# Performance work log

Measured on AMD Instinct MI355X. Metric: run time of the kernel, lower is better.

## Reference

```python
import jax, jax.numpy as jnp
import numpy as np

N = 50000   # nodes
E = 800000  # edges (avg degree 16)
G = 64      # graphs in batch
H = 4       # attention heads
D = 128     # hidden dim per head (= hidden_dim)
V = 128     # embedding vocab (input_dim)
NEG_SLOPE = 0.2

def setup_inputs() -> dict:
    key = jax.random.key(0)
    ks = jax.random.split(key, 12)
    s = 0.05
    return {
        "feats": jax.random.randint(ks[0], (N,), 0, V),
        "src": jax.random.randint(ks[1], (E,), 0, N),
        "dst": jax.random.randint(ks[2], (E,), 0, N),
        "graph_ids": jnp.sort(jax.random.randint(ks[3], (N,), 0, G)),
        "emb": jax.random.normal(ks[4], (V, D)) * s,
        "W1": jax.random.normal(ks[5], (D, H * D)) * s,
        "b1": jax.random.normal(ks[6], (H * D,)) * s,
        "a1": jax.random.normal(ks[7], (H, D)) * s,
        "W2": jax.random.normal(ks[8], (D, H * D)) * s,
        "b2": jax.random.normal(ks[9], (H * D,)) * s,
        "a2": jax.random.normal(ks[10], (H, D)) * s,
        "Wreg": jax.random.normal(ks[11], (1, D)) * s,
    }

def gatv2_layer(x, W, b, a, src, dst):
    # shared-weight GATv2: h = Wx + b, split into heads -> [N,H,D]
    h = (x @ W + b).reshape(-1, H, D)
    hs = h[src]                      # [E,H,D] source feats per edge
    hd = h[dst]                      # [E,H,D] dest feats per edge
    e = jax.nn.leaky_relu(hs + hd, NEG_SLOPE)
    logits = jnp.einsum('ehd,hd->eh', e, a)          # [E,H]
    # edge softmax over incoming edges of each dst node
    m = jax.ops.segment_max(logits, dst, num_segments=N)
    m = jnp.where(jnp.isfinite(m), m, 0.0)           # empty segments -> 0 (unused)
    ex = jnp.exp(logits - m[dst])
    denom = jax.ops.segment_sum(ex, dst, num_segments=N)
    alpha = ex / denom[dst]                          # [E,H]
    rst = jax.ops.segment_sum(alpha[:, :, None] * hs, dst, num_segments=N)  # [N,H,D]
    return rst.mean(axis=1)          # .mean(dim=1) over heads -> [N,D]

def reference(feats, src, dst, graph_ids, emb, W1, b1, a1, W2, b2, a2, Wreg):
    x = emb[feats]                                   # embedding lookup [N,D]
    x = gatv2_layer(x, W1, b1, a1, src, dst)         # layer 1 (dropout=0)
    x = gatv2_layer(x, W2, b2, a2, src, dst)         # layer 2
    pooled = jax.ops.segment_sum(x, graph_ids, num_segments=G)  # SumPooling [G,D]
    return pooled @ Wreg.T                           # Linear bias=False -> [G,1]
```

## Files before the change

### kernel.cpp

```cpp
#include <hip/hip_runtime.h>
#include <hip/hip_bf16.h>

#define N_NODES 50000
#define N_EDGES 800000
#define G_GRAPHS 64
#define H_HEADS 4
#define D_DIM 128
#define HD 512
#define V_VOCAB 128
#define NEG_SLOPE 0.2f

typedef float f32x2v __attribute__((ext_vector_type(2)));
typedef float f32x4 __attribute__((ext_vector_type(4)));
typedef short s16x8 __attribute__((ext_vector_type(8)));
typedef _Float16 h16x2 __attribute__((ext_vector_type(2)));

static __device__ __forceinline__ unsigned short f2b(float f) {
    union { float f; unsigned int i; } x; x.f = f;
    unsigned int r = x.i + 0x7fffu + ((x.i >> 16) & 1u);
    return (unsigned short)(r >> 16);
}
static __device__ __forceinline__ h16x2 u2h2(unsigned int u) {
    union { unsigned int u; h16x2 h; } c; c.u = u; return c.h;
}
static __device__ __forceinline__ unsigned int h22u(h16x2 h) {
    union { unsigned int u; h16x2 h; } c; c.h = h; return c.u;
}
static __device__ __forceinline__ h16x2 packf2(float lo, float hi) {
    union { __fp16 __attribute__((ext_vector_type(2))) p; h16x2 h; } c;
    c.p = __builtin_amdgcn_cvt_pkrtz(lo, hi);
    return c.h;
}

#if __has_builtin(__builtin_amdgcn_cvt_scalef32_pk_f16_fp8)
static __device__ __forceinline__ void fp8x4_to_h16(unsigned int u, h16x2& h0, h16x2& h1) {
    auto r0 = __builtin_amdgcn_cvt_scalef32_pk_f16_fp8((int)u, 1.0f, false);
    auto r1 = __builtin_amdgcn_cvt_scalef32_pk_f16_fp8((int)u, 1.0f, true);
    union { decltype(r0) p; h16x2 h; } c0, c1;
    c0.p = r0; c1.p = r1;
    h0 = c0.h; h1 = c1.h;
}
#else
static __device__ __forceinline__ void fp8x4_to_h16(unsigned int u, h16x2& h0, h16x2& h1) {
    f32x2v lo = __builtin_amdgcn_cvt_pk_f32_fp8(u, false);
    f32x2v hi = __builtin_amdgcn_cvt_pk_f32_fp8(u, true);
    h0 = packf2(lo.x, lo.y);
    h1 = packf2(hi.x, hi.y);
}
#endif

template<int CTRL>
static __device__ __forceinline__ float dpp_add(float v) {
    union { float f; int i; } a, b;
    a.f = v;
    b.i = __builtin_amdgcn_mov_dpp(a.i, CTRL, 0xF, 0xF, true);
    return v + b.f;
}
static __device__ __forceinline__ float row16_sum(float p) {
    p = dpp_add<0xB1>(p);
    p = dpp_add<0x4E>(p);
    p = dpp_add<0x141>(p);
    p = dpp_add<0x140>(p);
    return p;
}

#define MEGA_M1_BLOCKS   64
#define MEGA_WSZ_BLOCKS  256
#define MEGA_HIST_BLOCKS ((N_EDGES + 255) / 256)
__global__ void __launch_bounds__(256) mega_kernel(const float* __restrict__ emb,
                                                   const float* __restrict__ W1,
                                                   const float* __restrict__ b1,
                                                   unsigned int* __restrict__ M1b,
                                                   const float* __restrict__ W2,
                                                   unsigned short* __restrict__ Wb,
                                                   const int* __restrict__ dst,
                                                   int* __restrict__ counts,
                                                   float* __restrict__ pool) {
    int b = blockIdx.x;
    if (b < MEGA_M1_BLOCKS) {
        int idx = b * 256 + threadIdx.x;
        int v = idx >> 7, c0 = (idx & 127) * 4;
        float acc[4] = {b1[c0], b1[c0 + 1], b1[c0 + 2], b1[c0 + 3]};
        for (int k = 0; k < 128; k++) {
            float e = emb[v * 128 + k];
            #pragma unroll
            for (int j = 0; j < 4; j++) acc[j] = fmaf(e, W1[k * 512 + c0 + j], acc[j]);
        }
        unsigned int pk = __builtin_amdgcn_cvt_pk_fp8_f32(acc[0], acc[1], 0, false);
        pk = __builtin_amdgcn_cvt_pk_fp8_f32(acc[2], acc[3], pk, true);
        M1b[idx] = pk;
    } else if (b < MEGA_M1_BLOCKS + MEGA_WSZ_BLOCKS) {
        int idx = (b - MEGA_M1_BLOCKS) * 256 + threadIdx.x;
        int j = idx & 7, c = (idx >> 3) & 511, qq = idx >> 12;
        Wb[idx] = f2b(W2[(qq * 8 + j) * 512 + c]);
    } else {
        int hb = b - MEGA_M1_BLOCKS - MEGA_WSZ_BLOCKS;
        if (hb == 0 && threadIdx.x < G_GRAPHS) pool[threadIdx.x] = 0.f;
        int i = hb * 256 + threadIdx.x;
        if (i < N_EDGES) atomicAdd(&counts[dst[i]], 1);
    }
}

__global__ void __launch_bounds__(256) wtab_kernel(const unsigned int* __restrict__ M1b,
                                                   const float* __restrict__ a,
                                                   float* __restrict__ Wtab) {
    int wid = threadIdx.x >> 6, lane = threadIdx.x & 63;
    int pid = blockIdx.x * 4 + wid;
    int fd = pid >> 7, fs = pid & 127;
    int voff = lane * 2;

    h16x2 a06[4], a04[4], hd2[4], hs[4];
    float4 av0 = *reinterpret_cast<const float4*>(&a[lane * 8]);
    float4 av1 = *reinterpret_cast<const float4*>(&a[lane * 8 + 4]);
    float aa[8] = {av0.x, av0.y, av0.z, av0.w, av1.x, av1.y, av1.z, av1.w};
    const float L2E = 1.4426950408889634f;
    #pragma unroll
    for (int k = 0; k < 4; k++) {
        a06[k][0] = (_Float16)(aa[2*k]   * (0.6f * L2E));
        a06[k][1] = (_Float16)(aa[2*k+1] * (0.6f * L2E));
        a04[k][0] = (_Float16)(aa[2*k]   * (0.4f * L2E));
        a04[k][1] = (_Float16)(aa[2*k+1] * (0.4f * L2E));
    }
    uint2 hv = *reinterpret_cast<const uint2*>(&M1b[(unsigned)fd * 128u + voff]);
    fp8x4_to_h16(hv.x, hd2[0], hd2[1]);
    fp8x4_to_h16(hv.y, hd2[2], hd2[3]);
    uint2 sv = *reinterpret_cast<const uint2*>(&M1b[(unsigned)fs * 128u + voff]);
    fp8x4_to_h16(sv.x, hs[0], hs[1]);
    fp8x4_to_h16(sv.y, hs[2], hs[3]);

    float p = 0.f;
    #pragma unroll
    for (int k = 0; k < 4; k++) {
        h16x2 t2 = hs[k] + hd2[k];
        h16x2 at2 = u2h2(h22u(t2) & 0x7FFF7FFFu);
        p = __builtin_amdgcn_fdot2(t2, a06[k], p, false);
        p = __builtin_amdgcn_fdot2(at2, a04[k], p, false);
    }
    p = row16_sum(p);
    const float C1 = 0.69314718f, C2 = 0.24022651f, C3 = 0.05550411f;
    float w = fmaf(p, fmaf(p, fmaf(p, C3, C2), C1), 1.f);
    if ((lane & 15) == 0) Wtab[pid * 4 + (lane >> 4)] = w;
}

__global__ void __launch_bounds__(256) scanf_kernel(const int* __restrict__ counts,
                                                    int* __restrict__ offsets,
                                                    int* __restrict__ cursor,
                                                    int* __restrict__ bsum,
                                                    int* __restrict__ flag) {
    __shared__ int buf[256];
    __shared__ int sbase;
    int t = threadIdx.x, b = blockIdx.x;
    int i0 = (b * 256 + t) * 4;
    int v[4], c[4], s = 0;
    #pragma unroll
    for (int j = 0; j < 4; j++) {
        int idx = i0 + j;
        v[j] = (idx < N_NODES) ? counts[idx] : 0;
        s += v[j];
        c[j] = s;
    }
    buf[t] = s;
    __syncthreads();
    for (int off = 1; off < 256; off <<= 1) {
        int add = (t >= off) ? buf[t - off] : 0;
        __syncthreads();
        buf[t] += add;
        __syncthreads();
    }
    int ebase = (t > 0) ? buf[t - 1] : 0;
    if (t == 0) {
        bsum[b] = buf[255];
        __threadfence();
        atomicAdd(flag, 1);
        while (atomicAdd(flag, 0) < 64) __builtin_amdgcn_s_sleep(8);
    }
    __syncthreads();
    if (t < 64) {
        int vv = (t < b) ? atomicAdd(&bsum[t], 0) : 0;
        #pragma unroll
        for (int off = 1; off < 64; off <<= 1) vv += __shfl_xor(vv, off);
        if (t == 0) sbase = vv;
    }
    __syncthreads();
    int base = sbase;
    #pragma unroll
    for (int j = 0; j < 4; j++) {
        int idx = i0 + j;
        if (idx < N_NODES) {
            int e = base + ebase + c[j];
            offsets[idx + 1] = e;
            cursor[idx] = e - v[j];
        }
    }
    if (b == 0 && t == 0) offsets[0] = 0;
}

__global__ void scatter_kernel(const int* __restrict__ src, const int* __restrict__ dst,
                               int* __restrict__ cursor, int* __restrict__ csr_src) {
    int i = blockIdx.x * blockDim.x + threadIdx.x;
    if (i < N_EDGES) {
        int d = dst[i];
        int pos = atomicAdd(&cursor[d], 1);
        csr_src[pos] = src[i];
    }
}

template<bool LAYER1>
__global__ void __launch_bounds__(256) gat_kernel(const unsigned int* __restrict__ h,
                                                  const int* __restrict__ offsets,
                                                  const int* __restrict__ csr_src,
                                                  const int* __restrict__ feats,
                                                  const float* __restrict__ a,
                                                  const float* __restrict__ wreg,
                                                  const float* __restrict__ Wtab,
                                                  unsigned short* __restrict__ x,
                                                  float* __restrict__ dots) {
    int wid = threadIdx.x >> 6;
    int lane = threadIdx.x & 63;
    int n = blockIdx.x * 4 + wid;
    if (n >= N_NODES) return;
    n = __builtin_amdgcn_readfirstlane(n);
    int row_s = __builtin_amdgcn_readfirstlane(offsets[n]);
    int row_e = __builtin_amdgcn_readfirstlane(offsets[n + 1]);
    int cnt = row_e - row_s;
    int voff = lane * 2;

    auto ldrow = [&](int s) {
        return *reinterpret_cast<const uint2*>(&h[(unsigned)s * 128u + voff]);
    };

    if constexpr (LAYER1) {
        int fd = __builtin_amdgcn_readfirstlane(feats[n]);
        const float* wrow = &Wtab[fd * 512];
        int woff = lane >> 4;
        h16x2 acc2[4];
        #pragma unroll
        for (int k = 0; k < 4; k++) { acc2[k][0] = (_Float16)0.f; acc2[k][1] = (_Float16)0.f; }
        float den = 0.f;

        auto proc = [&](uint2 sv, float wv) {
            h16x2 hs[4];
            fp8x4_to_h16(sv.x, hs[0], hs[1]);
            fp8x4_to_h16(sv.y, hs[2], hs[3]);
            den += wv;
            h16x2 w2 = packf2(wv, wv);
            #pragma unroll
            for (int k = 0; k < 4; k++) acc2[k] = w2 * hs[k] + acc2[k];
        };

        for (int base = 0; base < cnt; base += 64) {
            int m = min(64, cnt - base);
            int ev = 0;
            if (lane < m) ev = feats[csr_src[row_s + base + lane]];
            int s0 = __builtin_amdgcn_readlane(ev, 0);
            int s1 = __builtin_amdgcn_readlane(ev, m > 1 ? 1 : 0);
            uint2 rA = ldrow(s0), rB = ldrow(s1);
            float wA = wrow[s0 * 4 + woff], wB = wrow[s1 * 4 + woff];
            for (int i = 0; i < m; i += 2) {
                {
                    uint2 c = rA; float wc = wA;
                    int sn = __builtin_amdgcn_readlane(ev, min(i + 2, m - 1));
                    rA = ldrow(sn); wA = wrow[sn * 4 + woff];
                    proc(c, wc);
                }
                if (i + 1 < m) {
                    uint2 c = rB; float wc = wB;
                    int sn = __builtin_amdgcn_readlane(ev, min(i + 3, m - 1));
                    rB = ldrow(sn); wB = wrow[sn * 4 + woff];
                    proc(c, wc);
                }
            }
        }

        float inv = (den > 0.f) ? 0.25f / den : 0.f;
        float out8[8];
        #pragma unroll
        for (int j = 0; j < 8; j++) {
            float r = (float)acc2[j >> 1][j & 1] * inv;
            r += __shfl_xor(r, 16);
            r += __shfl_xor(r, 32);
            out8[j] = r;
        }
        if (lane < 16) {
            union { unsigned short u[8]; uint4 v; } o;
            #pragma unroll
            for (int j = 0; j < 8; j++) o.u[j] = f2b(out8[j]);
            *reinterpret_cast<uint4*>(&x[(unsigned)n * 128u + lane * 8]) = o.v;
        }
        return;
    } else {
        h16x2 hd2[4], a06[4], a04[4], acc2[4];
        float pd;
        {
            uint2 hv = ldrow(n);
            fp8x4_to_h16(hv.x, hd2[0], hd2[1]);
            fp8x4_to_h16(hv.y, hd2[2], hd2[3]);
            float4 av0 = *reinterpret_cast<const float4*>(&a[lane * 8]);
            float4 av1 = *reinterpret_cast<const float4*>(&a[lane * 8 + 4]);
            float aa[8] = {av0.x, av0.y, av0.z, av0.w, av1.x, av1.y, av1.z, av1.w};
            const float L2E = 1.4426950408889634f;
            #pragma unroll
            for (int k = 0; k < 4; k++) {
                a06[k][0] = (_Float16)(aa[2*k]   * (0.6f * L2E));
                a06[k][1] = (_Float16)(aa[2*k+1] * (0.6f * L2E));
                a04[k][0] = (_Float16)(aa[2*k]   * (0.4f * L2E));
                a04[k][1] = (_Float16)(aa[2*k+1] * (0.4f * L2E));
                acc2[k][0] = (_Float16)0.f; acc2[k][1] = (_Float16)0.f;
            }
            float s = 0.f;
            #pragma unroll
            for (int k = 0; k < 4; k++) s = __builtin_amdgcn_fdot2(hd2[k], a06[k], s, false);
            pd = row16_sum(s);
        }

        const float C1 = 0.69314718f, C2 = 0.24022651f, C3 = 0.05550411f;
        float den = 0.f;

        auto process = [&](uint2 sv) {
            h16x2 hs[4];
            fp8x4_to_h16(sv.x, hs[0], hs[1]);
            fp8x4_to_h16(sv.y, hs[2], hs[3]);
            float p0 = 0.f, p1 = 0.f;
            #pragma unroll
            for (int k = 0; k < 2; k++) {
                h16x2 t2 = hs[k] + hd2[k];
                h16x2 at2 = u2h2(h22u(t2) & 0x7FFF7FFFu);
                p0 = __builtin_amdgcn_fdot2(hs[k], a06[k], p0, false);
                p0 = __builtin_amdgcn_fdot2(at2, a04[k], p0, false);
            }
            #pragma unroll
            for (int k = 2; k < 4; k++) {
                h16x2 t2 = hs[k] + hd2[k];
                h16x2 at2 = u2h2(h22u(t2) & 0x7FFF7FFFu);
                p1 = __builtin_amdgcn_fdot2(hs[k], a06[k], p1, false);
                p1 = __builtin_amdgcn_fdot2(at2, a04[k], p1, false);
            }
            float p = row16_sum(p0 + p1) + pd;
            float w = fmaf(p, fmaf(p, fmaf(p, C3, C2), C1), 1.f);
            den += w;
            h16x2 w2 = packf2(w, w);
            #pragma unroll
            for (int k = 0; k < 4; k++) acc2[k] = w2 * hs[k] + acc2[k];
        };

        for (int base = 0; base < cnt; base += 64) {
            int m = min(64, cnt - base);
            int ev = 0;
            if (lane < m) ev = csr_src[row_s + base + lane];
            int s0 = __builtin_amdgcn_readlane(ev, 0);
            int s1 = __builtin_amdgcn_readlane(ev, m > 1 ? 1 : 0);
            uint2 rA = ldrow(s0), rB = ldrow(s1);
            for (int i = 0; i < m; i += 2) {
                {
                    uint2 cur = rA;
                    rA = ldrow(__builtin_amdgcn_readlane(ev, min(i + 2, m - 1)));
                    process(cur);
                }
                if (i + 1 < m) {
                    uint2 cur = rB;
                    rB = ldrow(__builtin_amdgcn_readlane(ev, min(i + 3, m - 1)));
                    process(cur);
                }
            }
        }

        float inv = (den > 0.f) ? 0.25f / den : 0.f;
        float out8[8];
        #pragma unroll
        for (int j = 0; j < 8; j++) {
            float r = (float)acc2[j >> 1][j & 1] * inv;
            r += __shfl_xor(r, 16);
            r += __shfl_xor(r, 32);
            out8[j] = r;
        }
        int d0 = (lane & 15) * 8;
        float4 wv0 = *reinterpret_cast<const float4*>(&wreg[d0]);
        float4 wv1 = *reinterpret_cast<const float4*>(&wreg[d0 + 4]);
        float pdot = out8[0] * wv0.x + out8[1] * wv0.y + out8[2] * wv0.z + out8[3] * wv0.w
                   + out8[4] * wv1.x + out8[5] * wv1.y + out8[6] * wv1.z + out8[7] * wv1.w;
        pdot = row16_sum(pdot);
        if (lane == 0) dots[n] = pdot;
    }
}

__global__ void __launch_bounds__(256) gemm_kernel(const unsigned short* __restrict__ x,
                                                   const unsigned short* __restrict__ Wb,
                                                   const float* __restrict__ bias,
                                                   unsigned char* __restrict__ hout) {
    int w = threadIdx.x >> 6, l = threadIdx.x & 63;
    int rb = blockIdx.y * 64 + w * 16;
    int cb = blockIdx.x * 64;
    int lr = l & 15, lq = l >> 4;
    f32x4 acc[4] = {};
    int arow = rb + lr;
    bool rok = arow < N_NODES;
    #pragma unroll
    for (int s = 0; s < 4; s++) {
        s16x8 afr = {};
        if (rok) afr = *reinterpret_cast<const s16x8*>(&x[(size_t)arow * 128 + s * 32 + lq * 8]);
        #pragma unroll
        for (int sub = 0; sub < 4; sub++) {
            s16x8 bfr = *reinterpret_cast<const s16x8*>(
                &Wb[(((size_t)(s * 4 + lq) * 512) + cb + sub * 16 + lr) << 3]);
            acc[sub] = __builtin_amdgcn_mfma_f32_16x16x32_bf16(bfr, afr, acc[sub], 0, 0, 0);
        }
    }
    if (!rok) return;
    #pragma unroll
    for (int sub = 0; sub < 4; sub++) {
        int col0 = cb + sub * 16 + lq * 4;
        float4 bb = *reinterpret_cast<const float4*>(&bias[col0]);
        unsigned int pk = __builtin_amdgcn_cvt_pk_fp8_f32(acc[sub][0] + bb.x,
                                                          acc[sub][1] + bb.y, 0, false);
        pk = __builtin_amdgcn_cvt_pk_fp8_f32(acc[sub][2] + bb.z,
                                             acc[sub][3] + bb.w, pk, true);
        *reinterpret_cast<unsigned int*>(&hout[(size_t)arow * 512 + col0]) = pk;
    }
}

__global__ void __launch_bounds__(256) pool64_kernel(const float* __restrict__ dots,
                                                     const int* __restrict__ gid,
                                                     float* __restrict__ pool,
                                                     int* __restrict__ done,
                                                     float* __restrict__ out) {
    int wave = (blockIdx.x * blockDim.x + threadIdx.x) >> 6;
    int lane = threadIdx.x & 63;
    int n0 = wave * 64;
    if (n0 < N_NODES) {
        int n = n0 + lane;
        int nc = min(n, N_NODES - 1);
        int g = gid[nc];
        float v = (n < N_NODES) ? dots[n] : 0.f;
        int g0 = __shfl(g, 0);
        bool uni = __all(g == g0);
        if (uni) {
            v += __shfl_xor(v, 1);
            v += __shfl_xor(v, 2);
            v += __shfl_xor(v, 4);
            v += __shfl_xor(v, 8);
            v += __shfl_xor(v, 16);
            v += __shfl_xor(v, 32);
            if (lane == 0) atomicAdd(&pool[g0], v);
        } else {
            if (n < N_NODES) atomicAdd(&pool[g], v);
        }
    }
    __threadfence();
    __syncthreads();
    __shared__ int amlast;
    if (threadIdx.x == 0)
        amlast = (atomicAdd(done, 1) == (int)gridDim.x - 1) ? 1 : 0;
    __syncthreads();
    if (amlast && threadIdx.x < G_GRAPHS) {
        out[threadIdx.x] = atomicAdd(&pool[threadIdx.x], 0.f);
    }
}

extern "C" void kernel_launch(void* const* d_in, const int* in_sizes, int n_in,
                              void* d_out, int out_size, void* d_ws, size_t ws_size,
                              hipStream_t stream) {
    const int* feats = (const int*)d_in[0];
    const int* src   = (const int*)d_in[1];
    const int* dst   = (const int*)d_in[2];
    const int* gids  = (const int*)d_in[3];
    const float* emb  = (const float*)d_in[4];
    const float* W1   = (const float*)d_in[5];
    const float* b1   = (const float*)d_in[6];
    const float* a1   = (const float*)d_in[7];
    const float* W2   = (const float*)d_in[8];
    const float* b2   = (const float*)d_in[9];
    const float* a2   = (const float*)d_in[10];
    const float* wreg = (const float*)d_in[11];
    float* out = (float*)d_out;

    char* ws = (char*)d_ws;
    size_t off = 0;
    auto alloc = [&](size_t bytes) -> void* {
        void* p = ws + off;
        off = (off + bytes + 255) & ~(size_t)255;
        return p;
    };
    int*   counts  = (int*)alloc((size_t)N_NODES * 4 + 8);
    int*   flag    = counts + N_NODES;
    int*   done    = counts + N_NODES + 1;
    int*   offsets = (int*)alloc((size_t)(N_NODES + 1) * 4);
    int*   cursor  = (int*)alloc((size_t)N_NODES * 4);
    int*   csr_src = (int*)alloc((size_t)N_EDGES * 4);
    int*   bsum    = (int*)alloc(64 * 4);
    unsigned int*   M1b = (unsigned int*)alloc((size_t)V_VOCAB * HD);
    unsigned int*   h  = (unsigned int*)alloc((size_t)N_NODES * HD);
    unsigned short* x  = (unsigned short*)alloc((size_t)N_NODES * D_DIM * 2);
    unsigned short* Wb = (unsigned short*)alloc((size_t)D_DIM * HD * 2);
    float* Wtab    = (float*)alloc((size_t)V_VOCAB * V_VOCAB * H_HEADS * 4);
    float* dots    = (float*)alloc((size_t)N_NODES * 4);
    float* pool    = (float*)alloc((size_t)G_GRAPHS * 4);

    hipMemsetAsync(counts, 0, (size_t)N_NODES * 4 + 8, stream);

    mega_kernel<<<MEGA_M1_BLOCKS + MEGA_WSZ_BLOCKS + MEGA_HIST_BLOCKS, 256, 0, stream>>>(
        emb, W1, b1, M1b, W2, Wb, dst, counts, pool);
    wtab_kernel<<<(V_VOCAB * V_VOCAB) / 4, 256, 0, stream>>>(M1b, a1, Wtab);
    scanf_kernel<<<64, 256, 0, stream>>>(counts, offsets, cursor, bsum, flag);
    scatter_kernel<<<(N_EDGES + 255) / 256, 256, 0, stream>>>(src, dst, cursor, csr_src);

    gat_kernel<true><<<(N_NODES + 3) / 4, 256, 0, stream>>>(M1b, offsets, csr_src, feats,
                                                            a1, wreg, Wtab, x, dots);
    gemm_kernel<<<dim3(8, (N_NODES + 63) / 64), 256, 0, stream>>>(x, Wb, b2, (unsigned char*)h);
    gat_kernel<false><<<(N_NODES + 3) / 4, 256, 0, stream>>>(h, offsets, csr_src, feats,
                                                             a2, wreg, Wtab, x, dots);

    pool64_kernel<<<(N_NODES / 64 + 4) / 4, 256, 0, stream>>>(dots, gids, pool, done, out);
}
```

Before: 307.6 us.

## Precompute per-node score and readout projections to shrink layer-2 edge work

```diff
diff --git a/kernel.cpp b/kernel.cpp
--- a/kernel.cpp
+++ b/kernel.cpp
@@ -205,13 +205,50 @@
     }
 }
 
+__global__ void __launch_bounds__(256) pq_kernel(const unsigned int* __restrict__ h,
+                                                 const float* __restrict__ a,
+                                                 const float* __restrict__ wreg,
+                                                 float2* __restrict__ pq) {
+    int wid = threadIdx.x >> 6, lane = threadIdx.x & 63;
+    int n = blockIdx.x * 4 + wid;
+    if (n >= N_NODES) return;
+    int voff = lane * 2;
+    const float L2E = 1.4426950408889634f;
+
+    h16x2 a06[4], wf[4], hs[4];
+    float4 av0 = *reinterpret_cast<const float4*>(&a[lane * 8]);
+    float4 av1 = *reinterpret_cast<const float4*>(&a[lane * 8 + 4]);
+    float aa[8] = {av0.x, av0.y, av0.z, av0.w, av1.x, av1.y, av1.z, av1.w};
+    int d0 = (lane & 15) * 8;
+    float4 wv0 = *reinterpret_cast<const float4*>(&wreg[d0]);
+    float4 wv1 = *reinterpret_cast<const float4*>(&wreg[d0 + 4]);
+    float ww[8] = {wv0.x, wv0.y, wv0.z, wv0.w, wv1.x, wv1.y, wv1.z, wv1.w};
+    #pragma unroll
+    for (int k = 0; k < 4; k++) {
+        a06[k] = packf2(aa[2*k] * (0.6f * L2E), aa[2*k+1] * (0.6f * L2E));
+        wf[k]  = packf2(ww[2*k], ww[2*k+1]);
+    }
+    uint2 hv = *reinterpret_cast<const uint2*>(&h[(unsigned)n * 128u + voff]);
+    fp8x4_to_h16(hv.x, hs[0], hs[1]);
+    fp8x4_to_h16(hv.y, hs[2], hs[3]);
+    float ps = 0.f, q = 0.f;
+    #pragma unroll
+    for (int k = 0; k < 4; k++) {
+        ps = __builtin_amdgcn_fdot2(hs[k], a06[k], ps, false);
+        q  = __builtin_amdgcn_fdot2(hs[k], wf[k], q, false);
+    }
+    ps = row16_sum(ps);
+    q = row16_sum(q);
+    if ((lane & 15) == 0) pq[n * 4 + (lane >> 4)] = make_float2(ps, q);
+}
+
 template<bool LAYER1>
 __global__ void __launch_bounds__(256) gat_kernel(const unsigned int* __restrict__ h,
                                                   const int* __restrict__ offsets,
                                                   const int* __restrict__ csr_src,
                                                   const int* __restrict__ feats,
                                                   const float* __restrict__ a,
-                                                  const float* __restrict__ wreg,
+                                                  const float2* __restrict__ pq,
                                                   const float* __restrict__ Wtab,
                                                   unsigned short* __restrict__ x,
                                                   float* __restrict__ dots) {
@@ -289,7 +326,8 @@
         }
         return;
     } else {
-        h16x2 hd2[4], a06[4], a04[4], acc2[4];
+        int woff = lane >> 4;
+        h16x2 hd2[4], a04[4];
         float pd;
         {
             uint2 hv = ldrow(n);
@@ -300,47 +338,29 @@
             float aa[8] = {av0.x, av0.y, av0.z, av0.w, av1.x, av1.y, av1.z, av1.w};
             const float L2E = 1.4426950408889634f;
             #pragma unroll
-            for (int k = 0; k < 4; k++) {
-                a06[k][0] = (_Float16)(aa[2*k]   * (0.6f * L2E));
-                a06[k][1] = (_Float16)(aa[2*k+1] * (0.6f * L2E));
-                a04[k][0] = (_Float16)(aa[2*k]   * (0.4f * L2E));
-                a04[k][1] = (_Float16)(aa[2*k+1] * (0.4f * L2E));
-                acc2[k][0] = (_Float16)0.f; acc2[k][1] = (_Float16)0.f;
-            }
-            float s = 0.f;
-            #pragma unroll
-            for (int k = 0; k < 4; k++) s = __builtin_amdgcn_fdot2(hd2[k], a06[k], s, false);
-            pd = row16_sum(s);
+            for (int k = 0; k < 4; k++)
+                a04[k] = packf2(aa[2*k] * (0.4f * L2E), aa[2*k+1] * (0.4f * L2E));
+            pd = pq[n * 4 + woff].x;
         }
 
         const float C1 = 0.69314718f, C2 = 0.24022651f, C3 = 0.05550411f;
-        float den = 0.f;
-
-        auto process = [&](uint2 sv) {
+        float den = 0.f, num = 0.f;
+
+        auto process = [&](uint2 sv, float2 pqc) {
             h16x2 hs[4];
             fp8x4_to_h16(sv.x, hs[0], hs[1]);
             fp8x4_to_h16(sv.y, hs[2], hs[3]);
-            float p0 = 0.f, p1 = 0.f;
+            float p04 = 0.f;
             #pragma unroll
-            for (int k = 0; k < 2; k++) {
+            for (int k = 0; k < 4; k++) {
                 h16x2 t2 = hs[k] + hd2[k];
                 h16x2 at2 = u2h2(h22u(t2) & 0x7FFF7FFFu);
-                p0 = __builtin_amdgcn_fdot2(hs[k], a06[k], p0, false);
-                p0 = __builtin_amdgcn_fdot2(at2, a04[k], p0, false);
+                p04 = __builtin_amdgcn_fdot2(at2, a04[k], p04, false);
             }
-            #pragma unroll
-            for (int k = 2; k < 4; k++) {
-                h16x2 t2 = hs[k] + hd2[k];
-                h16x2 at2 = u2h2(h22u(t2) & 0x7FFF7FFFu);
-                p1 = __builtin_amdgcn_fdot2(hs[k], a06[k], p1, false);
-                p1 = __builtin_amdgcn_fdot2(at2, a04[k], p1, false);
-            }
-            float p = row16_sum(p0 + p1) + pd;
+            float p = row16_sum(p04) + pqc.x + pd;
             float w = fmaf(p, fmaf(p, fmaf(p, C3, C2), C1), 1.f);
             den += w;
-            h16x2 w2 = packf2(w, w);
-            #pragma unroll
-            for (int k = 0; k < 4; k++) acc2[k] = w2 * hs[k] + acc2[k];
+            num = fmaf(w, pqc.y, num);
         };
 
         for (int base = 0; base < cnt; base += 64) {
@@ -350,36 +370,27 @@
             int s0 = __builtin_amdgcn_readlane(ev, 0);
             int s1 = __builtin_amdgcn_readlane(ev, m > 1 ? 1 : 0);
             uint2 rA = ldrow(s0), rB = ldrow(s1);
+            float2 pA = pq[s0 * 4 + woff], pB = pq[s1 * 4 + woff];
             for (int i = 0; i < m; i += 2) {
                 {
-                    uint2 cur = rA;
-                    rA = ldrow(__builtin_amdgcn_readlane(ev, min(i + 2, m - 1)));
-                    process(cur);
+                    uint2 cur = rA; float2 pqc = pA;
+                    int sn = __builtin_amdgcn_readlane(ev, min(i + 2, m - 1));
+                    rA = ldrow(sn); pA = pq[sn * 4 + woff];
+                    process(cur, pqc);
                 }
                 if (i + 1 < m) {
-                    uint2 cur = rB;
-                    rB = ldrow(__builtin_amdgcn_readlane(ev, min(i + 3, m - 1)));
-                    process(cur);
+                    uint2 cur = rB; float2 pqc = pB;
+                    int sn = __builtin_amdgcn_readlane(ev, min(i + 3, m - 1));
+                    rB = ldrow(sn); pB = pq[sn * 4 + woff];
+                    process(cur, pqc);
                 }
             }
         }
 
-        float inv = (den > 0.f) ? 0.25f / den : 0.f;
-        float out8[8];
-        #pragma unroll
-        for (int j = 0; j < 8; j++) {
-            float r = (float)acc2[j >> 1][j & 1] * inv;
-            r += __shfl_xor(r, 16);
-            r += __shfl_xor(r, 32);
-            out8[j] = r;
-        }
-        int d0 = (lane & 15) * 8;
-        float4 wv0 = *reinterpret_cast<const float4*>(&wreg[d0]);
-        float4 wv1 = *reinterpret_cast<const float4*>(&wreg[d0 + 4]);
-        float pdot = out8[0] * wv0.x + out8[1] * wv0.y + out8[2] * wv0.z + out8[3] * wv0.w
-                   + out8[4] * wv1.x + out8[5] * wv1.y + out8[6] * wv1.z + out8[7] * wv1.w;
-        pdot = row16_sum(pdot);
-        if (lane == 0) dots[n] = pdot;
+        float r = (den > 0.f) ? num / den : 0.f;
+        r += __shfl_xor(r, 16);
+        r += __shfl_xor(r, 32);
+        if (lane == 0) dots[n] = 0.25f * r;
     }
 }
 
@@ -492,6 +503,7 @@
     unsigned short* x  = (unsigned short*)alloc((size_t)N_NODES * D_DIM * 2);
     unsigned short* Wb = (unsigned short*)alloc((size_t)D_DIM * HD * 2);
     float* Wtab    = (float*)alloc((size_t)V_VOCAB * V_VOCAB * H_HEADS * 4);
+    float2* pq     = (float2*)alloc((size_t)N_NODES * H_HEADS * 8);
     float* dots    = (float*)alloc((size_t)N_NODES * 4);
     float* pool    = (float*)alloc((size_t)G_GRAPHS * 4);
 
@@ -504,10 +516,11 @@
     scatter_kernel<<<(N_EDGES + 255) / 256, 256, 0, stream>>>(src, dst, cursor, csr_src);
 
     gat_kernel<true><<<(N_NODES + 3) / 4, 256, 0, stream>>>(M1b, offsets, csr_src, feats,
-                                                            a1, wreg, Wtab, x, dots);
+                                                            a1, pq, Wtab, x, dots);
     gemm_kernel<<<dim3(8, (N_NODES + 63) / 64), 256, 0, stream>>>(x, Wb, b2, (unsigned char*)h);
+    pq_kernel<<<(N_NODES + 3) / 4, 256, 0, stream>>>(h, a2, wreg, pq);
     gat_kernel<false><<<(N_NODES + 3) / 4, 256, 0, stream>>>(h, offsets, csr_src, feats,
-                                                             a2, wreg, Wtab, x, dots);
+                                                             a2, pq, Wtab, x, dots);
 
     pool64_kernel<<<(N_NODES / 64 + 4) / 4, 256, 0, stream>>>(dots, gids, pool, done, out);
 }
```

After: 312.2 us. Within noise of the previous version (+1.5%).
